# Performance work log

Measured on AMD Instinct MI355X. Metric: run time of the kernel, lower is better.

## Reference

```python
import jax, jax.numpy as jnp
import numpy as np

N_NODES = 32768
N_EDGES = 524288
NODE_DIM = 128
HIDDEN = 256
EDGE_DIM = 32


def setup_inputs() -> dict:
    key = jax.random.key(0)
    ks = jax.random.split(key, 12)
    s = 0.05
    return {
        "h": jax.random.normal(ks[0], (N_NODES, NODE_DIM), jnp.float32),
        "x": jax.random.normal(ks[1], (N_NODES, 3), jnp.float32) * 10.0,
        "edge_index": jax.random.randint(ks[2], (2, N_EDGES), 0, N_NODES, dtype=jnp.int32).astype(jnp.int64),
        "edge_dist": jax.random.uniform(ks[3], (N_EDGES,), jnp.float32) * 15.0,
        # edge_mlp: Linear(1, edge_dim) -> SiLU -> Linear(edge_dim, edge_dim)
        "We1": jax.random.normal(ks[4], (1, EDGE_DIM), jnp.float32) * s,
        "be1": jnp.zeros((EDGE_DIM,), jnp.float32),
        "We2": jax.random.normal(ks[5], (EDGE_DIM, EDGE_DIM), jnp.float32) * s,
        "be2": jnp.zeros((EDGE_DIM,), jnp.float32),
        # node_mlp: Linear(2*node+edge, hidden) -> SiLU -> Linear(hidden, node)
        "Wn1": jax.random.normal(ks[6], (2 * NODE_DIM + EDGE_DIM, HIDDEN), jnp.float32) * s,
        "bn1": jnp.zeros((HIDDEN,), jnp.float32),
        "Wn2": jax.random.normal(ks[7], (HIDDEN, NODE_DIM), jnp.float32) * s,
        "bn2": jnp.zeros((NODE_DIM,), jnp.float32),
        # coord_mlp: Linear(2*node+edge, hidden) -> SiLU -> Linear(hidden, 1, bias=False)
        "Wc1": jax.random.normal(ks[8], (2 * NODE_DIM + EDGE_DIM, HIDDEN), jnp.float32) * s,
        "bc1": jnp.zeros((HIDDEN,), jnp.float32),
        "Wc2": jax.random.normal(ks[9], (HIDDEN, 1), jnp.float32) * s,
    }


def reference(h, x, edge_index, edge_dist,
              We1, be1, We2, be2,
              Wn1, bn1, Wn2, bn2,
              Wc1, bc1, Wc2):
    src, dst = edge_index[0], edge_index[1]
    n_nodes = h.shape[0]

    # edge_mlp on scalar distances -> [E, edge_dim]
    edge_attr = jax.nn.silu(edge_dist[:, None] @ We1 + be1) @ We2 + be2

    # per-edge message input: [E, 2*node_dim + edge_dim]
    m_input = jnp.concatenate([h[src], h[dst], edge_attr], axis=-1)

    # node messages and scatter-add onto destination nodes
    m = jax.nn.silu(m_input @ Wn1 + bn1) @ Wn2 + bn2          # [E, node_dim]
    h_agg = jax.ops.segment_sum(m, dst, num_segments=n_nodes)  # [N, node_dim]

    # equivariant coordinate update along normalized edge direction
    coord_weight = jax.nn.silu(m_input @ Wc1 + bc1) @ Wc2      # [E, 1]
    dir_vec = x[src] - x[dst]                                  # [E, 3]
    dir_len = jnp.maximum(jnp.linalg.norm(dir_vec, axis=-1, keepdims=True), 1e-8)
    coord_update = coord_weight * (dir_vec / dir_len)          # [E, 3]
    x_agg = jax.ops.segment_sum(coord_update, dst, num_segments=n_nodes)

    return h + h_agg, x + x_agg
```

## Files before the change

### kernel.cpp

```cpp
#include <hip/hip_runtime.h>
#include <math.h>

#define N_NODES 32768
#define N_EDGES 524288
#define NODE_DIM 128
#define HIDDEN 256
#define EDGE_DIM 32
#define TE 32
#define NBLK (N_EDGES / TE)
#define ASTR 296
#define HSTR 264
#define MSTR 132

typedef __attribute__((ext_vector_type(8))) short bf16x8;
typedef __attribute__((ext_vector_type(16))) float f32x16;

__device__ __forceinline__ float silu_f(float v) {
    float e = __expf(-v);
    return v * __builtin_amdgcn_rcpf(1.0f + e);
}

__device__ __forceinline__ unsigned short f2bf_rne(float f) {
    union { float f; unsigned int u; } v; v.f = f;
    return (unsigned short)((v.u + 0x7fffu + ((v.u >> 16) & 1u)) >> 16);
}
__device__ __forceinline__ unsigned int pk_rne(float a, float b) {
    return (unsigned int)f2bf_rne(a) | ((unsigned int)f2bf_rne(b) << 16);
}
__device__ __forceinline__ unsigned int pkbf(float a, float b) {
    union { float f; unsigned int u; } ua, ub; ua.f = a; ub.f = b;
    return __builtin_amdgcn_perm(ub.u + 0x8000u, ua.u + 0x8000u, 0x07060302u);
}
__device__ __forceinline__ unsigned short f2bf_hu(float f) {
    union { float f; unsigned int u; } v; v.f = f;
    return (unsigned short)((v.u + 0x8000u) >> 16);
}

__device__ __forceinline__ int detect_is64(const void* ei, int t) {
    const unsigned int* ew = (const unsigned int*)ei;
    unsigned int hiw = ew[2 * (t & 63) + 1];
    return (__ballot(hiw != 0u) == 0ULL) ? 1 : 0;
}

#define WS_BIAS_OFF 1024
#define WS_W1S_OFF  69632
#define WS_W2S_OFF  364544
#define WS_CNT_OFF  430080
#define WS_CUR_OFF  561152
#define WS_PERM_OFF 692224
#define WS_PART_OFF 2789376
#define WS_HBF_OFF  2790400
#define WS_HBF_END  (WS_HBF_OFF + N_NODES * NODE_DIM * 2)

#define SEG_CNT  32768
#define SEG_W1S  147456
#define SEG_W2S  32768
#define SEG_BIAS 512
#define SEG_OUT  1073152
#define SEG_HBF  524288
#define PREP_TOT (SEG_CNT + SEG_W1S + SEG_W2S + SEG_BIAS + SEG_OUT + SEG_HBF)

__global__ void prep_all_kernel(const float* __restrict__ h, const float* __restrict__ x,
                                const float* __restrict__ We2, const float* __restrict__ be2,
                                const float* __restrict__ Wn1, const float* __restrict__ bn1,
                                const float* __restrict__ Wn2,
                                const float* __restrict__ Wc1, const float* __restrict__ bc1,
                                float* __restrict__ out, float* __restrict__ biasC,
                                unsigned short* __restrict__ W1s, unsigned short* __restrict__ W2s,
                                int* __restrict__ counts, unsigned short* __restrict__ hbf) {
    int i = blockIdx.x * 256 + threadIdx.x;
    if (i < SEG_CNT) { counts[i] = 0; return; }
    i -= SEG_CNT;
    if (i < SEG_W1S) {
        int jj = i & 7, ln = (i >> 3) & 63, rest = i >> 9;
        int step = rest % 18, tile = rest / 18;
        int n = tile * 32 + (ln & 31);
        int k = step * 16 + ((ln >> 5) * 8) + jj;
        float v;
        if (k < 256) {
            v = (n < 256) ? Wn1[k * 256 + n] : Wc1[k * 256 + (n - 256)];
        } else {
            int j = k - 256;
            float s = 0.0f;
            #pragma unroll 8
            for (int q = 0; q < 32; ++q)
                s += We2[j * 32 + q] * ((n < 256) ? Wn1[(256 + q) * 256 + n]
                                                  : Wc1[(256 + q) * 256 + (n - 256)]);
            v = s;
        }
        W1s[i] = f2bf_rne(v);
        return;
    }
    i -= SEG_W1S;
    if (i < SEG_W2S) {
        int jj = i & 7, ln = (i >> 3) & 63, rest = i >> 9;
        int step = rest & 15, tile = rest >> 4;
        int d = tile * 32 + (ln & 31);
        int k = step * 16 + ((ln >> 5) * 8) + jj;
        W2s[i] = f2bf_rne(Wn2[k * 128 + d]);
        return;
    }
    i -= SEG_W2S;
    if (i < SEG_BIAS) {
        int n = i;
        float s = (n < 256) ? bn1[n] : bc1[n - 256];
        #pragma unroll 8
        for (int q = 0; q < 32; ++q)
            s += be2[q] * ((n < 256) ? Wn1[(256 + q) * 256 + n]
                                     : Wc1[(256 + q) * 256 + (n - 256)]);
        biasC[n] = s;
        return;
    }
    i -= SEG_BIAS;
    if (i < SEG_OUT) {
        const int NH4 = N_NODES * NODE_DIM / 4;
        const float4* h4 = (const float4*)h;
        const float4* x4 = (const float4*)x;
        ((float4*)out)[i] = (i < NH4) ? h4[i] : x4[i - NH4];
        return;
    }
    i -= SEG_OUT;
    if (hbf != nullptr && i < SEG_HBF) {
        const float4* p = (const float4*)&h[i * 8];
        float4 v0 = p[0], v1 = p[1];
        uint4 o = make_uint4(pk_rne(v0.x, v0.y), pk_rne(v0.z, v0.w),
                             pk_rne(v1.x, v1.y), pk_rne(v1.z, v1.w));
        *(uint4*)&hbf[i * 8] = o;
    }
}

__global__ void hist_kernel(const void* __restrict__ ei, int* __restrict__ counts) {
    int is64 = detect_is64(ei, threadIdx.x);
    int e = blockIdx.x * 256 + threadIdx.x;
    int dst = is64 ? (int)((const long long*)ei)[N_EDGES + e]
                   : ((const int*)ei)[N_EDGES + e];
    atomicAdd(&counts[dst], 1);
}

__global__ __launch_bounds__(256)
void scanA_kernel(const int* __restrict__ counts, int* __restrict__ partials) {
    __shared__ int red[256];
    const int t = threadIdx.x;
    const int b = blockIdx.x;
    red[t] = counts[b * 256 + t];
    __syncthreads();
    #pragma unroll
    for (int s = 128; s > 0; s >>= 1) {
        if (t < s) red[t] += red[t + s];
        __syncthreads();
    }
    if (t == 0) partials[b] = red[0];
}

__global__ __launch_bounds__(256)
void scanC_kernel(const int* __restrict__ counts, const int* __restrict__ partials,
                  int* __restrict__ cursor) {
    __shared__ int pb[128];
    __shared__ int loc[256];
    const int t = threadIdx.x;
    const int b = blockIdx.x;
    if (t < 128) pb[t] = partials[t];
    int c = counts[b * 256 + t];
    loc[t] = c;
    __syncthreads();
    if (t == 0) {
        int s = 0;
        for (int j = 0; j < 128; ++j) { int v = pb[j]; pb[j] = s; s += v; }
    }
    #pragma unroll
    for (int d = 1; d < 256; d <<= 1) {
        int v = (t >= d) ? loc[t - d] : 0;
        __syncthreads();
        loc[t] += v;
        __syncthreads();
    }
    cursor[b * 256 + t] = pb[b] + loc[t] - c;
}

__global__ void place_kernel(const void* __restrict__ ei,
                             int* __restrict__ cursor, int* __restrict__ perm) {
    int is64 = detect_is64(ei, threadIdx.x);
    int e = blockIdx.x * 256 + threadIdx.x;
    int dst = is64 ? (int)((const long long*)ei)[N_EDGES + e]
                   : ((const int*)ei)[N_EDGES + e];
    int pos = atomicAdd(&cursor[dst], 1);
    perm[pos] = e;
}

__global__ __launch_bounds__(256, 4)
void egnn_mfma_kernel(const float* __restrict__ h, const float* __restrict__ x,
                      const void* __restrict__ ei, const float* __restrict__ dist,
                      const float* __restrict__ We1, const float* __restrict__ be1,
                      const float* __restrict__ bn2, const float* __restrict__ Wc2,
                      const float* __restrict__ biasC,
                      const unsigned short* __restrict__ W1s,
                      const unsigned short* __restrict__ W2s,
                      const int* __restrict__ perm,
                      const unsigned short* __restrict__ hbf,
                      float* __restrict__ out)
{
    __shared__ unsigned short smA[TE * ASTR];
    __shared__ int sidx[TE], didx[TE], eidx[TE];
    __shared__ float cw_s[TE];
    __shared__ float cxyz[3 * TE];

    unsigned short* smH = smA;
    float* smM = (float*)smA;

    const int t = threadIdx.x;
    const int lane = t & 63;
    const int wv = t >> 6;
    const int lo = lane & 31;
    const int hi = lane >> 5;
    const int swz = ((blockIdx.x & 7) * (NBLK / 8)) + (blockIdx.x >> 3);
    const int ebase = swz * TE;
    const int is64 = detect_is64(ei, t);

    if (t < 2 * TE) {
        int e = t & (TE - 1);
        int eid = perm[ebase + e];
        int which = t >> 5;
        long long pos = (long long)which * N_EDGES + eid;
        int idx = is64 ? (int)((const long long*)ei)[pos] : ((const int*)ei)[pos];
        if (which == 0) { sidx[e] = idx; eidx[e] = eid; }
        else didx[e] = idx;
        if (t < TE) cw_s[t] = 0.0f;
    }
    __syncthreads();

    if (hbf != nullptr) {
        #pragma unroll
        for (int it = 0; it < 4; ++it) {
            int id = it * 256 + t;
            int g = id & 15;
            int half = (id >> 4) & 1;
            int e = id >> 5;
            int node = half ? didx[e] : sidx[e];
            uint4 v = *(const uint4*)&hbf[node * NODE_DIM + 8 * g];
            *(uint4*)&smA[e * ASTR + half * NODE_DIM + 8 * g] = v;
        }
    } else {
        #pragma unroll
        for (int it = 0; it < 4; ++it) {
            int id = it * 256 + t;
            int g8 = id & 15;
            int half = (id >> 4) & 1;
            int e = id >> 5;
            int node = half ? didx[e] : sidx[e];
            const float4* p = (const float4*)&h[node * NODE_DIM + 8 * g8];
            float4 v0 = p[0], v1 = p[1];
            unsigned int a0 = pkbf(v0.x, v0.y), a1 = pkbf(v0.z, v0.w);
            unsigned int a2 = pkbf(v1.x, v1.y), a3 = pkbf(v1.z, v1.w);
            *(uint4*)&smA[e * ASTR + half * NODE_DIM + 8 * g8] = make_uint4(a0, a1, a2, a3);
        }
    }
    {
        int e = t >> 3;
        int j4 = (t & 7) * 4;
        float d = dist[eidx[e]];
        float s0 = silu_f(d * We1[j4 + 0] + be1[j4 + 0]);
        float s1 = silu_f(d * We1[j4 + 1] + be1[j4 + 1]);
        float s2 = silu_f(d * We1[j4 + 2] + be1[j4 + 2]);
        float s3 = silu_f(d * We1[j4 + 3] + be1[j4 + 3]);
        *(uint2*)&smA[e * ASTR + 2 * NODE_DIM + j4] = make_uint2(pkbf(s0, s1), pkbf(s2, s3));
    }
    if (t < TE) {
        int s = sidx[t], dn = didx[t];
        float dx = x[s * 3 + 0] - x[dn * 3 + 0];
        float dy = x[s * 3 + 1] - x[dn * 3 + 1];
        float dz = x[s * 3 + 2] - x[dn * 3 + 2];
        float len = fmaxf(sqrtf(dx * dx + dy * dy + dz * dz), 1e-8f);
        float inv = 1.0f / len;
        cxyz[t] = dx * inv; cxyz[TE + t] = dy * inv; cxyz[2 * TE + t] = dz * inv;
    }
    __syncthreads();

    f32x16 a0, a1, a2, a3;
    {
        float b0 = biasC[(wv     ) * 32 + lo];
        float b1 = biasC[(wv +  4) * 32 + lo];
        float b2 = biasC[(wv +  8) * 32 + lo];
        float b3 = biasC[(wv + 12) * 32 + lo];
        #pragma unroll
        for (int r = 0; r < 16; ++r) { a0[r] = b0; a1[r] = b1; a2[r] = b2; a3[r] = b3; }
    }
    {
        const int ao = lo * ASTR + hi * 8;
        const int TS = 18 * 64 * 8;
        const int b0 = (wv     ) * TS + lane * 8;
        const int b1 = (wv +  4) * TS + lane * 8;
        const int b2 = (wv +  8) * TS + lane * 8;
        const int b3 = (wv + 12) * TS + lane * 8;
        bf16x8 p0[2], p1[2], p2[2], p3[2];
        p0[0] = *(const bf16x8*)&W1s[b0];
        p1[0] = *(const bf16x8*)&W1s[b1];
        p2[0] = *(const bf16x8*)&W1s[b2];
        p3[0] = *(const bf16x8*)&W1s[b3];
        #pragma unroll
        for (int step = 0; step < 18; ++step) {
            const int cur = step & 1, nxt = cur ^ 1;
            if (step + 1 < 18) {
                p0[nxt] = *(const bf16x8*)&W1s[b0 + (step + 1) * 512];
                p1[nxt] = *(const bf16x8*)&W1s[b1 + (step + 1) * 512];
                p2[nxt] = *(const bf16x8*)&W1s[b2 + (step + 1) * 512];
                p3[nxt] = *(const bf16x8*)&W1s[b3 + (step + 1) * 512];
            }
            bf16x8 f = *(const bf16x8*)&smA[ao + step * 16];
            a0 = __builtin_amdgcn_mfma_f32_32x32x16_bf16(f, p0[cur], a0, 0, 0, 0);
            a1 = __builtin_amdgcn_mfma_f32_32x32x16_bf16(f, p1[cur], a1, 0, 0, 0);
            a2 = __builtin_amdgcn_mfma_f32_32x32x16_bf16(f, p2[cur], a2, 0, 0, 0);
            a3 = __builtin_amdgcn_mfma_f32_32x32x16_bf16(f, p3[cur], a3, 0, 0, 0);
        }
    }
    __syncthreads();

    const int rowbase = 4 * hi;
    {
        const int jb0 = (wv    ) * 32 + lo;
        const int jb1 = (wv + 4) * 32 + lo;
        #pragma unroll
        for (int r = 0; r < 16; ++r) {
            int er = (r & 3) + 8 * (r >> 2) + rowbase;
            smH[er * HSTR + jb0] = f2bf_hu(silu_f(a0[r]));
            smH[er * HSTR + jb1] = f2bf_hu(silu_f(a1[r]));
        }
        float w2 = Wc2[(wv    ) * 32 + lo];
        float w3 = Wc2[(wv + 4) * 32 + lo];
        float p[16];
        #pragma unroll
        for (int r = 0; r < 16; ++r)
            p[r] = silu_f(a2[r]) * w2 + silu_f(a3[r]) * w3;
        #pragma unroll
        for (int off = 1; off < 32; off <<= 1) {
            #pragma unroll
            for (int r = 0; r < 16; ++r) p[r] += __shfl_xor(p[r], off);
        }
        if (lo == 0) {
            #pragma unroll
            for (int r = 0; r < 16; ++r)
                atomicAdd(&cw_s[(r & 3) + 8 * (r >> 2) + rowbase], p[r]);
        }
    }
    __syncthreads();

    if (t < TE) {
        float w = cw_s[t];
        cxyz[t] *= w; cxyz[TE + t] *= w; cxyz[2 * TE + t] *= w;
    }

    {
        const int d = wv * 32 + lo;
        f32x16 acc;
        float bb = bn2[d];
        #pragma unroll
        for (int r = 0; r < 16; ++r) acc[r] = bb;
        const int hoff = lo * HSTR + hi * 8;
        const int wb = wv * (16 * 64 * 8) + lane * 8;
        bf16x8 bs[2];
        bs[0] = *(const bf16x8*)&W2s[wb];
        #pragma unroll
        for (int step = 0; step < 16; ++step) {
            const int cur = step & 1, nxt = cur ^ 1;
            if (step + 1 < 16)
                bs[nxt] = *(const bf16x8*)&W2s[wb + (step + 1) * 512];
            bf16x8 af = *(const bf16x8*)&smH[hoff + step * 16];
            acc = __builtin_amdgcn_mfma_f32_32x32x16_bf16(af, bs[cur], acc, 0, 0, 0);
        }
        __syncthreads();
        #pragma unroll
        for (int r = 0; r < 16; ++r) {
            int er = (r & 3) + 8 * (r >> 2) + rowbase;
            smM[er * MSTR + d] = acc[r];
        }
    }
    __syncthreads();

    {
        const int g = t >> 5;
        const int d4 = (t & 31) * 4;
        for (int e0 = g; e0 < TE; e0 += 8) {
            if (e0 > 0 && didx[e0] == didx[e0 - 1]) continue;
            float4 s = *(const float4*)&smM[e0 * MSTR + d4];
            int er = e0 + 1;
            while (er < TE && didx[er] == didx[e0]) {
                float4 v = *(const float4*)&smM[er * MSTR + d4];
                s.x += v.x; s.y += v.y; s.z += v.z; s.w += v.w;
                ++er;
            }
            float* dp = &out[didx[e0] * NODE_DIM + d4];
            if (e0 > 0 && er < TE) {
                float4 cur = *(const float4*)dp;
                cur.x += s.x; cur.y += s.y; cur.z += s.z; cur.w += s.w;
                *(float4*)dp = cur;
            } else {
                atomicAdd(dp + 0, s.x); atomicAdd(dp + 1, s.y);
                atomicAdd(dp + 2, s.z); atomicAdd(dp + 3, s.w);
            }
        }
    }
    if (t < TE) {
        int e0 = t;
        if (e0 == 0 || didx[e0] != didx[e0 - 1]) {
            float sx = cxyz[e0], sy = cxyz[TE + e0], sz = cxyz[2 * TE + e0];
            int er = e0 + 1;
            while (er < TE && didx[er] == didx[e0]) {
                sx += cxyz[er]; sy += cxyz[TE + er]; sz += cxyz[2 * TE + er];
                ++er;
            }
            float* xo = out + N_NODES * NODE_DIM + didx[e0] * 3;
            if (e0 > 0 && er < TE) {
                xo[0] += sx; xo[1] += sy; xo[2] += sz;
            } else {
                atomicAdd(xo + 0, sx); atomicAdd(xo + 1, sy); atomicAdd(xo + 2, sz);
            }
        }
    }
}

extern "C" void kernel_launch(void* const* d_in, const int* in_sizes, int n_in,
                              void* d_out, int out_size, void* d_ws, size_t ws_size,
                              hipStream_t stream) {
    const float* h    = (const float*)d_in[0];
    const float* x    = (const float*)d_in[1];
    const void*  ei   = d_in[2];
    const float* dist = (const float*)d_in[3];
    const float* We1  = (const float*)d_in[4];
    const float* be1  = (const float*)d_in[5];
    const float* We2  = (const float*)d_in[6];
    const float* be2  = (const float*)d_in[7];
    const float* Wn1  = (const float*)d_in[8];
    const float* bn1  = (const float*)d_in[9];
    const float* Wn2  = (const float*)d_in[10];
    const float* bn2  = (const float*)d_in[11];
    const float* Wc1  = (const float*)d_in[12];
    const float* bc1  = (const float*)d_in[13];
    const float* Wc2  = (const float*)d_in[14];
    float* out = (float*)d_out;

    float* biasC = (float*)((char*)d_ws + WS_BIAS_OFF);
    unsigned short* W1s = (unsigned short*)((char*)d_ws + WS_W1S_OFF);
    unsigned short* W2s = (unsigned short*)((char*)d_ws + WS_W2S_OFF);
    int* counts   = (int*)((char*)d_ws + WS_CNT_OFF);
    int* cursor   = (int*)((char*)d_ws + WS_CUR_OFF);
    int* perm     = (int*)((char*)d_ws + WS_PERM_OFF);
    int* partials = (int*)((char*)d_ws + WS_PART_OFF);
    unsigned short* hbf = (ws_size >= (size_t)WS_HBF_END)
                        ? (unsigned short*)((char*)d_ws + WS_HBF_OFF) : nullptr;

    prep_all_kernel<<<PREP_TOT / 256, 256, 0, stream>>>(
        h, x, We2, be2, Wn1, bn1, Wn2, Wc1, bc1,
        out, biasC, W1s, W2s, counts, hbf);

    hist_kernel<<<N_EDGES / 256, 256, 0, stream>>>(ei, counts);
    scanA_kernel<<<128, 256, 0, stream>>>(counts, partials);
    scanC_kernel<<<128, 256, 0, stream>>>(counts, partials, cursor);
    place_kernel<<<N_EDGES / 256, 256, 0, stream>>>(ei, cursor, perm);

    egnn_mfma_kernel<<<NBLK, 256, 0, stream>>>(
        h, x, ei, dist, We1, be1, bn2, Wc2, biasC, W1s, W2s, perm, hbf, out);
}
```

Measured before the change: 472.8 us.

## Precompute per-node destination term of first-layer GEMM and gather it per edge

Splits the first MLP layer so the h[dst] contribution is computed once per node (N×128×512 GEMM) in a new kernel and stored in bf16, then gathered per edge. Since edges are sorted by destination, the per-edge GEMM K shrinks from 288 to 160 and the shared-memory staging halves. The cost is an extra workspace buffer, an extra launch, gathered bf16 reads of the node term, and extra rounding of the precomputed term. The path only runs if the workspace is large enough.

```diff
diff --git a/kernel.cpp b/kernel.cpp
--- a/kernel.cpp
+++ b/kernel.cpp
@@ -9,6 +9,7 @@
 #define TE 32
 #define NBLK (N_EDGES / TE)
 #define ASTR 296
+#define A2STR 168
 #define HSTR 264
 #define MSTR 132
 
@@ -34,6 +35,10 @@
 __device__ __forceinline__ unsigned short f2bf_hu(float f) {
     union { float f; unsigned int u; } v; v.f = f;
     return (unsigned short)((v.u + 0x8000u) >> 16);
+}
+__device__ __forceinline__ float bfu(unsigned short u) {
+    union { unsigned int u; float f; } v; v.u = ((unsigned int)u) << 16;
+    return v.f;
 }
 
 __device__ __forceinline__ int detect_is64(const void* ei, int t) {
@@ -51,6 +56,8 @@
 #define WS_PART_OFF 2789376
 #define WS_HBF_OFF  2790400
 #define WS_HBF_END  (WS_HBF_OFF + N_NODES * NODE_DIM * 2)
+#define WS_NT_OFF   WS_HBF_END
+#define WS_NT_END   (WS_NT_OFF + N_NODES * 512 * 2)
 
 #define SEG_CNT  32768
 #define SEG_W1S  147456
@@ -60,6 +67,8 @@
 #define SEG_HBF  524288
 #define PREP_TOT (SEG_CNT + SEG_W1S + SEG_W2S + SEG_BIAS + SEG_OUT + SEG_HBF)
 
+#define W1SA_SH 81920
+
 __global__ void prep_all_kernel(const float* __restrict__ h, const float* __restrict__ x,
                                 const float* __restrict__ We2, const float* __restrict__ be2,
                                 const float* __restrict__ Wn1, const float* __restrict__ bn1,
@@ -67,28 +76,57 @@
                                 const float* __restrict__ Wc1, const float* __restrict__ bc1,
                                 float* __restrict__ out, float* __restrict__ biasC,
                                 unsigned short* __restrict__ W1s, unsigned short* __restrict__ W2s,
-                                int* __restrict__ counts, unsigned short* __restrict__ hbf) {
+                                int* __restrict__ counts, unsigned short* __restrict__ hbf,
+                                int use_nt) {
     int i = blockIdx.x * 256 + threadIdx.x;
     if (i < SEG_CNT) { counts[i] = 0; return; }
     i -= SEG_CNT;
     if (i < SEG_W1S) {
-        int jj = i & 7, ln = (i >> 3) & 63, rest = i >> 9;
-        int step = rest % 18, tile = rest / 18;
-        int n = tile * 32 + (ln & 31);
-        int k = step * 16 + ((ln >> 5) * 8) + jj;
-        float v;
-        if (k < 256) {
-            v = (n < 256) ? Wn1[k * 256 + n] : Wc1[k * 256 + (n - 256)];
+        if (!use_nt) {
+            int jj = i & 7, ln = (i >> 3) & 63, rest = i >> 9;
+            int step = rest % 18, tile = rest / 18;
+            int n = tile * 32 + (ln & 31);
+            int k = step * 16 + ((ln >> 5) * 8) + jj;
+            float v;
+            if (k < 256) {
+                v = (n < 256) ? Wn1[k * 256 + n] : Wc1[k * 256 + (n - 256)];
+            } else {
+                int j = k - 256;
+                float s = 0.0f;
+                #pragma unroll 8
+                for (int q = 0; q < 32; ++q)
+                    s += We2[j * 32 + q] * ((n < 256) ? Wn1[(256 + q) * 256 + n]
+                                                      : Wc1[(256 + q) * 256 + (n - 256)]);
+                v = s;
+            }
+            W1s[i] = f2bf_rne(v);
+        } else if (i < W1SA_SH) {
+            int jj = i & 7, ln = (i >> 3) & 63, rest = i >> 9;
+            int step = rest % 10, tile = rest / 10;
+            int n = tile * 32 + (ln & 31);
+            int k = step * 16 + ((ln >> 5) * 8) + jj;
+            float v;
+            if (k < 128) {
+                v = (n < 256) ? Wn1[k * 256 + n] : Wc1[k * 256 + (n - 256)];
+            } else {
+                int j = k - 128;
+                float s = 0.0f;
+                #pragma unroll 8
+                for (int q = 0; q < 32; ++q)
+                    s += We2[j * 32 + q] * ((n < 256) ? Wn1[(256 + q) * 256 + n]
+                                                      : Wc1[(256 + q) * 256 + (n - 256)]);
+                v = s;
+            }
+            W1s[i] = f2bf_rne(v);
         } else {
-            int j = k - 256;
-            float s = 0.0f;
-            #pragma unroll 8
-            for (int q = 0; q < 32; ++q)
-                s += We2[j * 32 + q] * ((n < 256) ? Wn1[(256 + q) * 256 + n]
-                                                  : Wc1[(256 + q) * 256 + (n - 256)]);
-            v = s;
-        }
-        W1s[i] = f2bf_rne(v);
+            int i2 = i - W1SA_SH;
+            int jj = i2 & 7, ln = (i2 >> 3) & 63, rest = i2 >> 9;
+            int step = rest & 7, tile = rest >> 3;
+            int n = tile * 32 + (ln & 31);
+            int kk = 128 + step * 16 + ((ln >> 5) * 8) + jj;
+            float v = (n < 256) ? Wn1[kk * 256 + n] : Wc1[kk * 256 + (n - 256)];
+            W1s[i] = f2bf_rne(v);
+        }
         return;
     }
     i -= SEG_W1S;
@@ -185,6 +223,282 @@
                    : ((const int*)ei)[N_EDGES + e];
     int pos = atomicAdd(&cursor[dst], 1);
     perm[pos] = e;
+}
+
+__global__ __launch_bounds__(256, 4)
+void nterm_kernel(const unsigned short* __restrict__ hbf,
+                  const unsigned short* __restrict__ W1sB,
+                  unsigned short* __restrict__ nt) {
+    const int t = threadIdx.x;
+    const int lane = t & 63;
+    const int wv = t >> 6;
+    const int lo = lane & 31;
+    const int hi = lane >> 5;
+    const int nb = blockIdx.x * 32;
+
+    f32x16 a0, a1, a2, a3;
+    #pragma unroll
+    for (int r = 0; r < 16; ++r) { a0[r] = 0.f; a1[r] = 0.f; a2[r] = 0.f; a3[r] = 0.f; }
+
+    const int aoff = (nb + lo) * NODE_DIM + hi * 8;
+    const int TSB = 8 * 64 * 8;
+    const int b0 = (wv     ) * TSB + lane * 8;
+    const int b1 = (wv +  4) * TSB + lane * 8;
+    const int b2 = (wv +  8) * TSB + lane * 8;
+    const int b3 = (wv + 12) * TSB + lane * 8;
+    bf16x8 p0[2], p1[2], p2[2], p3[2];
+    p0[0] = *(const bf16x8*)&W1sB[b0];
+    p1[0] = *(const bf16x8*)&W1sB[b1];
+    p2[0] = *(const bf16x8*)&W1sB[b2];
+    p3[0] = *(const bf16x8*)&W1sB[b3];
+    #pragma unroll
+    for (int step = 0; step < 8; ++step) {
+        const int cur = step & 1, nxt = cur ^ 1;
+        if (step + 1 < 8) {
+            p0[nxt] = *(const bf16x8*)&W1sB[b0 + (step + 1) * 512];
+            p1[nxt] = *(const bf16x8*)&W1sB[b1 + (step + 1) * 512];
+            p2[nxt] = *(const bf16x8*)&W1sB[b2 + (step + 1) * 512];
+            p3[nxt] = *(const bf16x8*)&W1sB[b3 + (step + 1) * 512];
+        }
+        bf16x8 f = *(const bf16x8*)&hbf[aoff + step * 16];
+        a0 = __builtin_amdgcn_mfma_f32_32x32x16_bf16(f, p0[cur], a0, 0, 0, 0);
+        a1 = __builtin_amdgcn_mfma_f32_32x32x16_bf16(f, p1[cur], a1, 0, 0, 0);
+        a2 = __builtin_amdgcn_mfma_f32_32x32x16_bf16(f, p2[cur], a2, 0, 0, 0);
+        a3 = __builtin_amdgcn_mfma_f32_32x32x16_bf16(f, p3[cur], a3, 0, 0, 0);
+    }
+    #pragma unroll
+    for (int r = 0; r < 16; ++r) {
+        int er = (r & 3) + 8 * (r >> 2) + 4 * hi;
+        unsigned short* row = &nt[(unsigned)(nb + er) * 512 + lo];
+        row[(wv     ) * 32] = f2bf_rne(a0[r]);
+        row[(wv +  4) * 32] = f2bf_rne(a1[r]);
+        row[(wv +  8) * 32] = f2bf_rne(a2[r]);
+        row[(wv + 12) * 32] = f2bf_rne(a3[r]);
+    }
+}
+
+__global__ __launch_bounds__(256, 4)
+void egnn_nt_kernel(const float* __restrict__ x,
+                    const void* __restrict__ ei, const float* __restrict__ dist,
+                    const float* __restrict__ We1, const float* __restrict__ be1,
+                    const float* __restrict__ bn2, const float* __restrict__ Wc2,
+                    const float* __restrict__ biasC,
+                    const unsigned short* __restrict__ W1s,
+                    const unsigned short* __restrict__ W2s,
+                    const int* __restrict__ perm,
+                    const unsigned short* __restrict__ hbf,
+                    const unsigned short* __restrict__ nt,
+                    float* __restrict__ out)
+{
+    __shared__ unsigned short smU[TE * HSTR];
+    __shared__ int sidx[TE], didx[TE], eidx[TE];
+    __shared__ float cw_s[TE];
+    __shared__ float cxyz[3 * TE];
+
+    unsigned short* smA = smU;
+    unsigned short* smH = smU;
+    float* smM = (float*)smU;
+
+    const int t = threadIdx.x;
+    const int lane = t & 63;
+    const int wv = t >> 6;
+    const int lo = lane & 31;
+    const int hi = lane >> 5;
+    const int swz = ((blockIdx.x & 7) * (NBLK / 8)) + (blockIdx.x >> 3);
+    const int ebase = swz * TE;
+    const int is64 = detect_is64(ei, t);
+
+    if (t < 2 * TE) {
+        int e = t & (TE - 1);
+        int eid = perm[ebase + e];
+        int which = t >> 5;
+        long long pos = (long long)which * N_EDGES + eid;
+        int idx = is64 ? (int)((const long long*)ei)[pos] : ((const int*)ei)[pos];
+        if (which == 0) { sidx[e] = idx; eidx[e] = eid; }
+        else didx[e] = idx;
+        if (t < TE) cw_s[t] = 0.0f;
+    }
+    __syncthreads();
+
+    #pragma unroll
+    for (int it = 0; it < 2; ++it) {
+        int id = it * 256 + t;
+        int g = id & 15;
+        int e = id >> 4;
+        int node = sidx[e];
+        uint4 v = *(const uint4*)&hbf[node * NODE_DIM + 8 * g];
+        *(uint4*)&smA[e * A2STR + 8 * g] = v;
+    }
+    {
+        int e = t >> 3;
+        int j4 = (t & 7) * 4;
+        float d = dist[eidx[e]];
+        float s0 = silu_f(d * We1[j4 + 0] + be1[j4 + 0]);
+        float s1 = silu_f(d * We1[j4 + 1] + be1[j4 + 1]);
+        float s2 = silu_f(d * We1[j4 + 2] + be1[j4 + 2]);
+        float s3 = silu_f(d * We1[j4 + 3] + be1[j4 + 3]);
+        *(uint2*)&smA[e * A2STR + NODE_DIM + j4] = make_uint2(pkbf(s0, s1), pkbf(s2, s3));
+    }
+    if (t < TE) {
+        int s = sidx[t], dn = didx[t];
+        float dx = x[s * 3 + 0] - x[dn * 3 + 0];
+        float dy = x[s * 3 + 1] - x[dn * 3 + 1];
+        float dz = x[s * 3 + 2] - x[dn * 3 + 2];
+        float len = fmaxf(sqrtf(dx * dx + dy * dy + dz * dz), 1e-8f);
+        float inv = 1.0f / len;
+        cxyz[t] = dx * inv; cxyz[TE + t] = dy * inv; cxyz[2 * TE + t] = dz * inv;
+    }
+    __syncthreads();
+
+    f32x16 a0, a1, a2, a3;
+    {
+        float b0 = biasC[(wv     ) * 32 + lo];
+        float b1 = biasC[(wv +  4) * 32 + lo];
+        float b2 = biasC[(wv +  8) * 32 + lo];
+        float b3 = biasC[(wv + 12) * 32 + lo];
+        #pragma unroll
+        for (int r = 0; r < 16; ++r) { a0[r] = b0; a1[r] = b1; a2[r] = b2; a3[r] = b3; }
+    }
+    {
+        const int ao = lo * A2STR + hi * 8;
+        const int TSA = 10 * 64 * 8;
+        const int b0 = (wv     ) * TSA + lane * 8;
+        const int b1 = (wv +  4) * TSA + lane * 8;
+        const int b2 = (wv +  8) * TSA + lane * 8;
+        const int b3 = (wv + 12) * TSA + lane * 8;
+        bf16x8 p0[2], p1[2], p2[2], p3[2];
+        p0[0] = *(const bf16x8*)&W1s[b0];
+        p1[0] = *(const bf16x8*)&W1s[b1];
+        p2[0] = *(const bf16x8*)&W1s[b2];
+        p3[0] = *(const bf16x8*)&W1s[b3];
+        #pragma unroll
+        for (int step = 0; step < 10; ++step) {
+            const int cur = step & 1, nxt = cur ^ 1;
+            if (step + 1 < 10) {
+                p0[nxt] = *(const bf16x8*)&W1s[b0 + (step + 1) * 512];
+                p1[nxt] = *(const bf16x8*)&W1s[b1 + (step + 1) * 512];
+                p2[nxt] = *(const bf16x8*)&W1s[b2 + (step + 1) * 512];
+                p3[nxt] = *(const bf16x8*)&W1s[b3 + (step + 1) * 512];
+            }
+            bf16x8 f = *(const bf16x8*)&smA[ao + step * 16];
+            a0 = __builtin_amdgcn_mfma_f32_32x32x16_bf16(f, p0[cur], a0, 0, 0, 0);
+            a1 = __builtin_amdgcn_mfma_f32_32x32x16_bf16(f, p1[cur], a1, 0, 0, 0);
+            a2 = __builtin_amdgcn_mfma_f32_32x32x16_bf16(f, p2[cur], a2, 0, 0, 0);
+            a3 = __builtin_amdgcn_mfma_f32_32x32x16_bf16(f, p3[cur], a3, 0, 0, 0);
+        }
+    }
+    __syncthreads();
+
+    const int rowbase = 4 * hi;
+    {
+        #pragma unroll
+        for (int r = 0; r < 16; ++r) {
+            int er = (r & 3) + 8 * (r >> 2) + rowbase;
+            const unsigned short* np = &nt[(unsigned)didx[er] * 512 + lo];
+            a0[r] += bfu(np[(wv     ) * 32]);
+            a1[r] += bfu(np[(wv +  4) * 32]);
+            a2[r] += bfu(np[(wv +  8) * 32]);
+            a3[r] += bfu(np[(wv + 12) * 32]);
+        }
+        const int jb0 = (wv    ) * 32 + lo;
+        const int jb1 = (wv + 4) * 32 + lo;
+        #pragma unroll
+        for (int r = 0; r < 16; ++r) {
+            int er = (r & 3) + 8 * (r >> 2) + rowbase;
+            smH[er * HSTR + jb0] = f2bf_hu(silu_f(a0[r]));
+            smH[er * HSTR + jb1] = f2bf_hu(silu_f(a1[r]));
+        }
+        float w2 = Wc2[(wv    ) * 32 + lo];
+        float w3 = Wc2[(wv + 4) * 32 + lo];
+        float p[16];
+        #pragma unroll
+        for (int r = 0; r < 16; ++r)
+            p[r] = silu_f(a2[r]) * w2 + silu_f(a3[r]) * w3;
+        #pragma unroll
+        for (int off = 1; off < 32; off <<= 1) {
+            #pragma unroll
+            for (int r = 0; r < 16; ++r) p[r] += __shfl_xor(p[r], off);
+        }
+        if (lo == 0) {
+            #pragma unroll
+            for (int r = 0; r < 16; ++r)
+                atomicAdd(&cw_s[(r & 3) + 8 * (r >> 2) + rowbase], p[r]);
+        }
+    }
+    __syncthreads();
+
+    if (t < TE) {
+        float w = cw_s[t];
+        cxyz[t] *= w; cxyz[TE + t] *= w; cxyz[2 * TE + t] *= w;
+    }
+
+    {
+        const int d = wv * 32 + lo;
+        f32x16 acc;
+        float bb = bn2[d];
+        #pragma unroll
+        for (int r = 0; r < 16; ++r) acc[r] = bb;
+        const int hoff = lo * HSTR + hi * 8;
+        const int wb = wv * (16 * 64 * 8) + lane * 8;
+        bf16x8 bs[2];
+        bs[0] = *(const bf16x8*)&W2s[wb];
+        #pragma unroll
+        for (int step = 0; step < 16; ++step) {
+            const int cur = step & 1, nxt = cur ^ 1;
+            if (step + 1 < 16)
+                bs[nxt] = *(const bf16x8*)&W2s[wb + (step + 1) * 512];
+            bf16x8 af = *(const bf16x8*)&smH[hoff + step * 16];
+            acc = __builtin_amdgcn_mfma_f32_32x32x16_bf16(af, bs[cur], acc, 0, 0, 0);
+        }
+        __syncthreads();
+        #pragma unroll
+        for (int r = 0; r < 16; ++r) {
+            int er = (r & 3) + 8 * (r >> 2) + rowbase;
+            smM[er * MSTR + d] = acc[r];
+        }
+    }
+    __syncthreads();
+
+    {
+        const int g = t >> 5;
+        const int d4 = (t & 31) * 4;
+        for (int e0 = g; e0 < TE; e0 += 8) {
+            if (e0 > 0 && didx[e0] == didx[e0 - 1]) continue;
+            float4 s = *(const float4*)&smM[e0 * MSTR + d4];
+            int er = e0 + 1;
+            while (er < TE && didx[er] == didx[e0]) {
+                float4 v = *(const float4*)&smM[er * MSTR + d4];
+                s.x += v.x; s.y += v.y; s.z += v.z; s.w += v.w;
+                ++er;
+            }
+            float* dp = &out[didx[e0] * NODE_DIM + d4];
+            if (e0 > 0 && er < TE) {
+                float4 cur = *(const float4*)dp;
+                cur.x += s.x; cur.y += s.y; cur.z += s.z; cur.w += s.w;
+                *(float4*)dp = cur;
+            } else {
+                atomicAdd(dp + 0, s.x); atomicAdd(dp + 1, s.y);
+                atomicAdd(dp + 2, s.z); atomicAdd(dp + 3, s.w);
+            }
+        }
+    }
+    if (t < TE) {
+        int e0 = t;
+        if (e0 == 0 || didx[e0] != didx[e0 - 1]) {
+            float sx = cxyz[e0], sy = cxyz[TE + e0], sz = cxyz[2 * TE + e0];
+            int er = e0 + 1;
+            while (er < TE && didx[er] == didx[e0]) {
+                sx += cxyz[er]; sy += cxyz[TE + er]; sz += cxyz[2 * TE + er];
+                ++er;
+            }
+            float* xo = out + N_NODES * NODE_DIM + didx[e0] * 3;
+            if (e0 > 0 && er < TE) {
+                xo[0] += sx; xo[1] += sy; xo[2] += sz;
+            } else {
+                atomicAdd(xo + 0, sx); atomicAdd(xo + 1, sy); atomicAdd(xo + 2, sz);
+            }
+        }
+    }
 }
 
 __global__ __launch_bounds__(256, 4)
@@ -446,16 +760,24 @@
     int* partials = (int*)((char*)d_ws + WS_PART_OFF);
     unsigned short* hbf = (ws_size >= (size_t)WS_HBF_END)
                         ? (unsigned short*)((char*)d_ws + WS_HBF_OFF) : nullptr;
+    int use_nt = (ws_size >= (size_t)WS_NT_END) ? 1 : 0;
+    unsigned short* nt = use_nt ? (unsigned short*)((char*)d_ws + WS_NT_OFF) : nullptr;
 
     prep_all_kernel<<<PREP_TOT / 256, 256, 0, stream>>>(
         h, x, We2, be2, Wn1, bn1, Wn2, Wc1, bc1,
-        out, biasC, W1s, W2s, counts, hbf);
+        out, biasC, W1s, W2s, counts, hbf, use_nt);
 
     hist_kernel<<<N_EDGES / 256, 256, 0, stream>>>(ei, counts);
     scanA_kernel<<<128, 256, 0, stream>>>(counts, partials);
     scanC_kernel<<<128, 256, 0, stream>>>(counts, partials, cursor);
     place_kernel<<<N_EDGES / 256, 256, 0, stream>>>(ei, cursor, perm);
 
-    egnn_mfma_kernel<<<NBLK, 256, 0, stream>>>(
-        h, x, ei, dist, We1, be1, bn2, Wc2, biasC, W1s, W2s, perm, hbf, out);
-}
+    if (use_nt) {
+        nterm_kernel<<<N_NODES / 32, 256, 0, stream>>>(hbf, W1s + W1SA_SH, nt);
+        egnn_nt_kernel<<<NBLK, 256, 0, stream>>>(
+            x, ei, dist, We1, be1, bn2, Wc2, biasC, W1s, W2s, perm, hbf, nt, out);
+    } else {
+        egnn_mfma_kernel<<<NBLK, 256, 0, stream>>>(
+            h, x, ei, dist, We1, be1, bn2, Wc2, biasC, W1s, W2s, perm, hbf, out);
+    }
+}
```

After: 568.2 us. 1.2x slower.

## Split first-layer MFMA into two passes to cut accumulator registers

Applied to the files above, without the earlier changes.

The fused first-layer GEMM kept four 32x32 accumulators live at once. It is now split so the coord-MLP half is computed and reduced to per-edge weights first, and the node-MLP half is computed afterwards. This lowers peak accumulator pressure so launch bounds can rise from 4 to 5 blocks per CU. One barrier is moved so the coordinate scaling sits before the second GEMM's sync. The cost is reloading the shared-memory A fragments twice, and the higher occupancy target could force register spills.

```diff
diff --git a/kernel.cpp b/kernel.cpp
--- a/kernel.cpp
+++ b/kernel.cpp
@@ -187,7 +187,7 @@
     perm[pos] = e;
 }
 
-__global__ __launch_bounds__(256, 4)
+__global__ __launch_bounds__(256, 5)
 void egnn_mfma_kernel(const float* __restrict__ h, const float* __restrict__ x,
                       const void* __restrict__ ei, const float* __restrict__ dist,
                       const float* __restrict__ We1, const float* __restrict__ be1,
@@ -275,46 +275,81 @@
     }
     __syncthreads();
 
-    f32x16 a0, a1, a2, a3;
-    {
-        float b0 = biasC[(wv     ) * 32 + lo];
-        float b1 = biasC[(wv +  4) * 32 + lo];
-        float b2 = biasC[(wv +  8) * 32 + lo];
-        float b3 = biasC[(wv + 12) * 32 + lo];
-        #pragma unroll
-        for (int r = 0; r < 16; ++r) { a0[r] = b0; a1[r] = b1; a2[r] = b2; a3[r] = b3; }
-    }
-    {
+    const int rowbase = 4 * hi;
+
+    {
+        f32x16 c0, c1;
+        {
+            float b0 = biasC[256 + wv * 32 + lo];
+            float b1 = biasC[256 + (wv + 4) * 32 + lo];
+            #pragma unroll
+            for (int r = 0; r < 16; ++r) { c0[r] = b0; c1[r] = b1; }
+        }
+        {
+            const int ao = lo * ASTR + hi * 8;
+            const int TS = 18 * 64 * 8;
+            const int q0 = (8 + wv) * TS + lane * 8;
+            const int q1 = (12 + wv) * TS + lane * 8;
+            bf16x8 p0[2], p1[2];
+            p0[0] = *(const bf16x8*)&W1s[q0];
+            p1[0] = *(const bf16x8*)&W1s[q1];
+            #pragma unroll
+            for (int step = 0; step < 18; ++step) {
+                const int cur = step & 1, nxt = cur ^ 1;
+                if (step + 1 < 18) {
+                    p0[nxt] = *(const bf16x8*)&W1s[q0 + (step + 1) * 512];
+                    p1[nxt] = *(const bf16x8*)&W1s[q1 + (step + 1) * 512];
+                }
+                bf16x8 f = *(const bf16x8*)&smA[ao + step * 16];
+                c0 = __builtin_amdgcn_mfma_f32_32x32x16_bf16(f, p0[cur], c0, 0, 0, 0);
+                c1 = __builtin_amdgcn_mfma_f32_32x32x16_bf16(f, p1[cur], c1, 0, 0, 0);
+            }
+        }
+        float w0 = Wc2[wv * 32 + lo];
+        float w1 = Wc2[(wv + 4) * 32 + lo];
+        float p[16];
+        #pragma unroll
+        for (int r = 0; r < 16; ++r)
+            p[r] = silu_f(c0[r]) * w0 + silu_f(c1[r]) * w1;
+        #pragma unroll
+        for (int off = 1; off < 32; off <<= 1) {
+            #pragma unroll
+            for (int r = 0; r < 16; ++r) p[r] += __shfl_xor(p[r], off);
+        }
+        if (lo == 0) {
+            #pragma unroll
+            for (int r = 0; r < 16; ++r)
+                atomicAdd(&cw_s[(r & 3) + 8 * (r >> 2) + rowbase], p[r]);
+        }
+    }
+
+    f32x16 a0, a1;
+    {
+        float b0 = biasC[wv * 32 + lo];
+        float b1 = biasC[(wv + 4) * 32 + lo];
+        #pragma unroll
+        for (int r = 0; r < 16; ++r) { a0[r] = b0; a1[r] = b1; }
         const int ao = lo * ASTR + hi * 8;
         const int TS = 18 * 64 * 8;
-        const int b0 = (wv     ) * TS + lane * 8;
-        const int b1 = (wv +  4) * TS + lane * 8;
-        const int b2 = (wv +  8) * TS + lane * 8;
-        const int b3 = (wv + 12) * TS + lane * 8;
-        bf16x8 p0[2], p1[2], p2[2], p3[2];
-        p0[0] = *(const bf16x8*)&W1s[b0];
-        p1[0] = *(const bf16x8*)&W1s[b1];
-        p2[0] = *(const bf16x8*)&W1s[b2];
-        p3[0] = *(const bf16x8*)&W1s[b3];
+        const int q0 = (wv) * TS + lane * 8;
+        const int q1 = (wv + 4) * TS + lane * 8;
+        bf16x8 p0[2], p1[2];
+        p0[0] = *(const bf16x8*)&W1s[q0];
+        p1[0] = *(const bf16x8*)&W1s[q1];
         #pragma unroll
         for (int step = 0; step < 18; ++step) {
             const int cur = step & 1, nxt = cur ^ 1;
             if (step + 1 < 18) {
-                p0[nxt] = *(const bf16x8*)&W1s[b0 + (step + 1) * 512];
-                p1[nxt] = *(const bf16x8*)&W1s[b1 + (step + 1) * 512];
-                p2[nxt] = *(const bf16x8*)&W1s[b2 + (step + 1) * 512];
-                p3[nxt] = *(const bf16x8*)&W1s[b3 + (step + 1) * 512];
+                p0[nxt] = *(const bf16x8*)&W1s[q0 + (step + 1) * 512];
+                p1[nxt] = *(const bf16x8*)&W1s[q1 + (step + 1) * 512];
             }
             bf16x8 f = *(const bf16x8*)&smA[ao + step * 16];
             a0 = __builtin_amdgcn_mfma_f32_32x32x16_bf16(f, p0[cur], a0, 0, 0, 0);
             a1 = __builtin_amdgcn_mfma_f32_32x32x16_bf16(f, p1[cur], a1, 0, 0, 0);
-            a2 = __builtin_amdgcn_mfma_f32_32x32x16_bf16(f, p2[cur], a2, 0, 0, 0);
-            a3 = __builtin_amdgcn_mfma_f32_32x32x16_bf16(f, p3[cur], a3, 0, 0, 0);
-        }
-    }
-    __syncthreads();
-
-    const int rowbase = 4 * hi;
+        }
+    }
+    __syncthreads();
+
     {
         const int jb0 = (wv    ) * 32 + lo;
         const int jb1 = (wv + 4) * 32 + lo;
@@ -324,29 +359,12 @@
             smH[er * HSTR + jb0] = f2bf_hu(silu_f(a0[r]));
             smH[er * HSTR + jb1] = f2bf_hu(silu_f(a1[r]));
         }
-        float w2 = Wc2[(wv    ) * 32 + lo];
-        float w3 = Wc2[(wv + 4) * 32 + lo];
-        float p[16];
-        #pragma unroll
-        for (int r = 0; r < 16; ++r)
-            p[r] = silu_f(a2[r]) * w2 + silu_f(a3[r]) * w3;
-        #pragma unroll
-        for (int off = 1; off < 32; off <<= 1) {
-            #pragma unroll
-            for (int r = 0; r < 16; ++r) p[r] += __shfl_xor(p[r], off);
-        }
-        if (lo == 0) {
-            #pragma unroll
-            for (int r = 0; r < 16; ++r)
-                atomicAdd(&cw_s[(r & 3) + 8 * (r >> 2) + rowbase], p[r]);
-        }
-    }
-    __syncthreads();
-
+    }
     if (t < TE) {
         float w = cw_s[t];
         cxyz[t] *= w; cxyz[TE + t] *= w; cxyz[2 * TE + t] *= w;
     }
+    __syncthreads();
 
     {
         const int d = wv * 32 + lo;
```

Measured after the change: 477.7 us. No clear change (+1.0%).
